# Performance work log

Measured on AMD Instinct MI355X. Metric: run time of the kernel, lower is better.

The kernel has to match this reference:

```python
import jax, jax.numpy as jnp
import numpy as np

EMBED_DIM = 1024
NUM_HEADS = 16
HEAD_DIM = EMBED_DIM // NUM_HEADS
ROPE_BASE = 10000.0
SQK_INIT_VALUE = 1.0
SQK_INIT_SCALING = 1.0 / (EMBED_DIM ** 0.5)


def setup_inputs() -> dict:
    key = jax.random.key(0)
    ks = jax.random.split(key, 6)
    B, N = 1, 2048
    x = jax.random.normal(ks[0], (B, N, EMBED_DIM), dtype=jnp.float32)
    # torch nn.Linear weights are [out_features, in_features]; y = x @ W.T
    s = EMBED_DIM ** -0.5
    Wq = jax.random.normal(ks[1], (EMBED_DIM, EMBED_DIM), dtype=jnp.float32) * s
    Wk = jax.random.normal(ks[2], (EMBED_DIM, EMBED_DIM), dtype=jnp.float32) * s
    Wv = jax.random.normal(ks[3], (EMBED_DIM, EMBED_DIM), dtype=jnp.float32) * s
    Wo = jax.random.normal(ks[4], (EMBED_DIM, EMBED_DIM), dtype=jnp.float32) * s
    sqk = SQK_INIT_SCALING * jnp.ones((EMBED_DIM,), dtype=jnp.float32) \
        + 0.01 * jax.random.normal(ks[5], (EMBED_DIM,), dtype=jnp.float32)
    return {"x": x, "Wq": Wq, "Wk": Wk, "Wv": Wv, "Wo": Wo, "sqk": sqk}


def _rope(t, offset=0):
    # t: [b, h, n, d]; rotary position embedding (Lrpe type 1), half-split layout
    d = t.shape[-1]
    n = t.shape[-2]
    inv_freq = 1.0 / (ROPE_BASE ** (jnp.arange(0, d, 2, dtype=jnp.float32) / d))  # [d/2]
    pos = jnp.arange(n, dtype=jnp.float32) + offset                               # [n]
    freqs = pos[:, None] * inv_freq[None, :]                                      # [n, d/2]
    cos = jnp.cos(freqs)
    sin = jnp.sin(freqs)
    t1, t2 = jnp.split(t, 2, axis=-1)
    return jnp.concatenate([t1 * cos - t2 * sin, t1 * sin + t2 * cos], axis=-1)


def _justnorm(t):
    return t / jnp.linalg.norm(t, axis=-1, keepdims=True)


def reference(x, Wq, Wk, Wv, Wo, sqk):
    B, N, E = x.shape
    H, D = NUM_HEADS, HEAD_DIM
    q = jnp.einsum('bne,fe->bnf', x, Wq).reshape(B, N, H, D).transpose(0, 2, 1, 3)
    k = jnp.einsum('bne,fe->bnf', x, Wk).reshape(B, N, H, D).transpose(0, 2, 1, 3)
    v = jnp.einsum('bne,fe->bnf', x, Wv).reshape(B, N, H, D).transpose(0, 2, 1, 3)
    q = _rope(q)
    k = _rope(k)
    # sqk * (init_value / init_scaling), reshaped to (h, 1, d)
    sqk_s = (sqk * (SQK_INIT_VALUE / SQK_INIT_SCALING)).reshape(H, 1, D)
    q = sqk_s * _justnorm(q)
    k = sqk_s * _justnorm(k)
    # SDPA with scale = sqrt(head_dim) (as in the source), causal
    scale = D ** 0.5
    scores = jnp.einsum('bhnd,bhmd->bhnm', q, k) * scale
    causal = jnp.tril(jnp.ones((N, N), dtype=bool))
    scores = jnp.where(causal, scores, -jnp.inf)
    attn = jax.nn.softmax(scores, axis=-1)
    out = jnp.einsum('bhnm,bhmd->bhnd', attn, v)           # [b,h,n,d]
    out = out.transpose(0, 2, 1, 3).reshape(B, N, E)       # [b,n,e]
    out = jnp.einsum('bne,fe->bnf', out, Wo)
    return out
```

## Files before the change

### kernel.cpp

```cpp
#include <hip/hip_runtime.h>
#include <hip/hip_bf16.h>

typedef float f32x4 __attribute__((ext_vector_type(4)));
typedef __bf16 bf16x8 __attribute__((ext_vector_type(8)));
typedef __bf16 bf16x4 __attribute__((ext_vector_type(4)));

__device__ __forceinline__ void gload_lds16(const __bf16* g, __bf16* l) {
  __builtin_amdgcn_global_load_lds(
      (const __attribute__((address_space(1))) void*)g,
      (__attribute__((address_space(3))) void*)l, 16, 0, 0);
}

__global__ __launch_bounds__(256) void convert_all(
    const float* __restrict__ x, const float* __restrict__ wq,
    const float* __restrict__ wk, const float* __restrict__ wv,
    const float* __restrict__ wo, __bf16* __restrict__ dst)
{
  int t = blockIdx.x * 256 + threadIdx.x;
  const float* src; size_t soff;
  if (t < 262144) { src = x; soff = (size_t)t * 8; }
  else {
    int r = (t - 262144) >> 17;
    src = (r == 0) ? wq : (r == 1) ? wk : (r == 2) ? wv : wo;
    soff = (size_t)((t - 262144) & 131071) * 8;
  }
  float4 f0 = *(const float4*)(src + soff);
  float4 f1 = *(const float4*)(src + soff + 4);
  bf16x8 o;
  o[0]=(__bf16)f0.x; o[1]=(__bf16)f0.y; o[2]=(__bf16)f0.z; o[3]=(__bf16)f0.w;
  o[4]=(__bf16)f1.x; o[5]=(__bf16)f1.y; o[6]=(__bf16)f1.z; o[7]=(__bf16)f1.w;
  *(bf16x8*)(dst + (size_t)t * 8) = o;
}

template <int BM, int BN, int BK, typename OutT, bool ROPE>
__global__ __launch_bounds__(256) void gemm_bt(
    const __bf16* __restrict__ A,
    const __bf16* __restrict__ B0, const __bf16* __restrict__ B1, const __bf16* __restrict__ B2,
    OutT* __restrict__ C0, OutT* __restrict__ C1, OutT* __restrict__ C2,
    int M, int N, int K, const float* __restrict__ sqkp)
{
  const __bf16* B = (blockIdx.z == 0) ? B0 : (blockIdx.z == 1) ? B1 : B2;
  OutT* C = (blockIdx.z == 0) ? C0 : (blockIdx.z == 1) ? C1 : C2;

  constexpr int MT = BM / 32, NT = BN / 32, KK = BK / 32;
  constexpr int CPR = BK / 8;
  constexpr int RPI = 64 / CPR;
  __shared__ __align__(16) __bf16 smem[BM * BK + BN * BK];
  __bf16* As = smem;
  __bf16* Bs = smem + BM * BK;

  const int tid = threadIdx.x, w = tid >> 6, l = tid & 63;
  const int wr = w >> 1, wc = w & 1;
  const int g = l >> 4, c16 = l & 15;
  const int bm = blockIdx.y, bn = blockIdx.x;
  const int lr = l / CPR, lc = l % CPR;

  f32x4 acc[MT][NT] = {};
  const int nk = K / BK;

  for (int kt = 0; kt < nk; ++kt) {
    __syncthreads();
#pragma unroll
    for (int i = w; i < BM / RPI; i += 4) {
      int row = i * RPI + lr;
      int sch = lc ^ (row & 7);
      gload_lds16(A + (size_t)(bm * BM + row) * K + kt * BK + sch * 8, As + i * RPI * BK);
    }
#pragma unroll
    for (int i = w; i < BN / RPI; i += 4) {
      int row = i * RPI + lr;
      int sch = lc ^ (row & 7);
      gload_lds16(B + (size_t)(bn * BN + row) * K + kt * BK + sch * 8, Bs + i * RPI * BK);
    }
    __syncthreads();

#pragma unroll
    for (int kk = 0; kk < KK; ++kk) {
      bf16x8 af[MT], bf[NT];
#pragma unroll
      for (int mt = 0; mt < MT; ++mt) {
        int row = wr * (BM / 2) + mt * 16 + c16;
        af[mt] = *(const bf16x8*)(As + row * BK + (((kk * 4 + g) ^ (row & 7)) * 8));
      }
#pragma unroll
      for (int nt = 0; nt < NT; ++nt) {
        int row = wc * (BN / 2) + nt * 16 + c16;
        bf[nt] = *(const bf16x8*)(Bs + row * BK + (((kk * 4 + g) ^ (row & 7)) * 8));
      }
#pragma unroll
      for (int mt = 0; mt < MT; ++mt)
#pragma unroll
        for (int nt = 0; nt < NT; ++nt)
          acc[mt][nt] = __builtin_amdgcn_mfma_f32_16x16x32_bf16(af[mt], bf[nt], acc[mt][nt], 0, 0, 0);
    }
  }

  bool done = false;
  if constexpr (ROPE) {
    static_assert(!ROPE || (NT == 4 && MT == 2), "ROPE kernel assumes BM=64, BN=128");
    if (blockIdx.z == 2) {
      __syncthreads();
#pragma unroll
      for (int mt = 0; mt < MT; ++mt)
#pragma unroll
        for (int nt = 0; nt < NT; ++nt) {
          bf16x4 pk;
#pragma unroll
          for (int r = 0; r < 4; ++r) pk[r] = (__bf16)acc[mt][nt][r];
          int n0 = wr * 32 + mt * 16 + g * 4;
          int d  = nt * 16 + c16;
          *(bf16x4*)(smem + wc * 4608 + d * 72 + n0) = pk;
        }
      __syncthreads();
#pragma unroll
      for (int j = 0; j < 4; ++j) {
        int idx = tid + j * 256;
        int head = idx >> 9;
        int rem = idx & 511;
        int d = rem >> 3;
        int c8 = (rem & 7) * 8;
        bf16x8 val = *(const bf16x8*)(smem + head * 4608 + d * 72 + c8);
        *(bf16x8*)(C + (size_t)((bn * 2 + head) * 64 + d) * 2048 + bm * 64 + c8) = val;
      }
      done = true;
    } else {
      const bool isQ = (blockIdx.z == 0);
      const int hcol = bn * BN + wc * (BN / 2);
      float sq[4];
#pragma unroll
      for (int nt = 0; nt < 4; ++nt) sq[nt] = sqkp[hcol + nt * 16 + c16] * 32.0f;
      const float QSC = 8.0f * 1.4426950408889634f;
      const float L = 0.415241011860919f;
      const float inv0 = exp2f(-(float)c16 * L);
      const float inv1 = exp2f(-(float)(c16 + 16) * L);
#pragma unroll
      for (int mt = 0; mt < MT; ++mt) {
#pragma unroll
        for (int r = 0; r < 4; ++r) {
          int row = bm * BM + wr * (BM / 2) + mt * 16 + g * 4 + r;
          float s0, c0, s1, c1;
          sincosf((float)row * inv0, &s0, &c0);
          sincosf((float)row * inv1, &s1, &c1);
          float v0 = acc[mt][0][r], v1 = acc[mt][1][r];
          float v2 = acc[mt][2][r], v3 = acc[mt][3][r];
          float n0 = v0 * c0 - v2 * s0;
          float n2 = v0 * s0 + v2 * c0;
          float n1 = v1 * c1 - v3 * s1;
          float n3 = v1 * s1 + v3 * c1;
          float ss = n0 * n0 + n1 * n1 + n2 * n2 + n3 * n3;
#pragma unroll
          for (int m2 = 1; m2 < 16; m2 <<= 1) ss += __shfl_xor(ss, m2, 16);
          float rinv = rsqrtf(ss);
          if (isQ) rinv *= QSC;
          C[(size_t)row * N + hcol +  0 + c16] = (OutT)(n0 * sq[0] * rinv);
          C[(size_t)row * N + hcol + 16 + c16] = (OutT)(n1 * sq[1] * rinv);
          C[(size_t)row * N + hcol + 32 + c16] = (OutT)(n2 * sq[2] * rinv);
          C[(size_t)row * N + hcol + 48 + c16] = (OutT)(n3 * sq[3] * rinv);
        }
      }
      done = true;
    }
  }
  if (!done) {
#pragma unroll
    for (int mt = 0; mt < MT; ++mt)
#pragma unroll
      for (int nt = 0; nt < NT; ++nt)
#pragma unroll
        for (int r = 0; r < 4; ++r) {
          int row = bm * BM + wr * (BM / 2) + mt * 16 + g * 4 + r;
          int col = bn * BN + wc * (BN / 2) + nt * 16 + c16;
          C[(size_t)row * N + col] = (OutT)acc[mt][nt][r];
        }
  }
}

#define STAGE(BUF, KT)                                                         \
  {                                                                            \
    _Pragma("unroll")                                                          \
    for (int p = 0; p < 2; ++p) {                                              \
      int row = srow + p * 32;                                                 \
      int sch = sc ^ (row & 7);                                                \
      gload_lds16(Kg + (size_t)((KT) * 64 + row) * 1024 + h * 64 + sch * 8,    \
                  &Ks[BUF][w * 512 + p * 2048]);                               \
      gload_lds16(Vg + ((size_t)h * 64 + row) * 2048 + (KT) * 64 + sch * 8,    \
                  &Vs[BUF][w * 512 + p * 2048]);                               \
    }                                                                          \
  }

__global__ __launch_bounds__(256, 4) void attn_kernel(
    const __bf16* __restrict__ Qg, const __bf16* __restrict__ Kg,
    const __bf16* __restrict__ Vg, __bf16* __restrict__ Og,
    float* __restrict__ oS, float* __restrict__ lS)
{
  __shared__ __align__(16) __bf16 Ks[2][4096];
  __shared__ __align__(16) __bf16 Vs[2][4096];
  __shared__ __align__(16) __bf16 Ps[4][16 * 72];

  const int b = blockIdx.x;
  int h, qt, kts, kte, sidx;
  if (b < 512) {
    int p = b >> 5;
    qt = 16 + p;
    sidx = (b >> 4) & 1;
    h = b & 15;
    int mid = (qt + 1) >> 1;
    kts = sidx ? mid : 0;
    kte = sidx ? qt : (mid - 1);
  } else {
    qt = 15 - ((b - 512) >> 4);
    h = b & 15;
    kts = 0; kte = qt; sidx = -1;
  }
  const int q0 = qt * 64;

  const int tid = threadIdx.x, w = tid >> 6, l = tid & 63;
  const int g = l >> 4, c16 = l & 15;
  const int srow = tid >> 3;
  const int sc   = tid & 7;

  __bf16* Ps_w = &Ps[w][0];
  const int qig = q0 + w * 16 + c16;

  const __bf16* qbase = Qg + (size_t)qig * 1024 + h * 64 + g * 8;
  const bf16x8 qf0 = *(const bf16x8*)(qbase);
  const bf16x8 qf1 = *(const bf16x8*)(qbase + 32);

  f32x4 o[4] = {};
  float lsum = 0.f;

  STAGE(0, kts)

  for (int kt = kts; kt <= kte; ++kt) {
    const int cur = (kt - kts) & 1;
    __syncthreads();
    if (kt < kte) STAGE(cur ^ 1, kt + 1)

    const __bf16* Kb = Ks[cur];
    const __bf16* Vb = Vs[cur];

    f32x4 s[4] = {};
#pragma unroll
    for (int kjb = 0; kjb < 4; ++kjb) {
      int r = kjb * 16 + c16;
      bf16x8 k0 = *(const bf16x8*)((char*)Kb + r * 128 + ((g ^ (r & 7)) * 16));
      bf16x8 k1 = *(const bf16x8*)((char*)Kb + r * 128 + (((4 + g) ^ (r & 7)) * 16));
      s[kjb] = __builtin_amdgcn_mfma_f32_16x16x32_bf16(k0, qf0, s[kjb], 0, 0, 0);
      s[kjb] = __builtin_amdgcn_mfma_f32_16x16x32_bf16(k1, qf1, s[kjb], 0, 0, 0);
    }

    const bool diag = (kt == qt);
#pragma unroll
    for (int kjb = 0; kjb < 4; ++kjb) {
      bf16x4 pk;
#pragma unroll
      for (int r = 0; r < 4; ++r) {
        float sv = s[kjb][r];
        int kvg = kt * 64 + kjb * 16 + g * 4 + r;
        if (diag && kvg > qig) sv = -1e30f;
        float e = exp2f(sv);
        pk[r] = (__bf16)e;
        lsum += e;
      }
      *(bf16x4*)((char*)Ps_w + c16 * 144 + kjb * 32 + g * 8) = pk;
    }

#pragma unroll
    for (int ks = 0; ks < 2; ++ks) {
      bf16x8 pa = *(const bf16x8*)((char*)Ps_w + c16 * 144 + ks * 64 + g * 16);
#pragma unroll
      for (int nt = 0; nt < 4; ++nt) {
        int r = nt * 16 + c16;
        bf16x8 vb = *(const bf16x8*)((char*)Vb + r * 128 + (((ks * 4 + g) ^ (r & 7)) * 16));
        o[nt] = __builtin_amdgcn_mfma_f32_16x16x32_bf16(pa, vb, o[nt], 0, 0, 0);
      }
    }
  }

  lsum += __shfl_xor(lsum, 16);
  lsum += __shfl_xor(lsum, 32);

  if (sidx < 0) {
    float* lsh = (float*)Ps_w;
    if (g == 0) lsh[c16] = lsum;
    __builtin_amdgcn_s_waitcnt(0);
#pragma unroll
    for (int r = 0; r < 4; ++r) {
      float rinv = 1.0f / lsh[g * 4 + r];
      int qi = q0 + w * 16 + g * 4 + r;
#pragma unroll
      for (int nt = 0; nt < 4; ++nt)
        Og[(size_t)qi * 1024 + h * 64 + nt * 16 + c16] = (__bf16)(o[nt][r] * rinv);
    }
  } else {
    float* oBase = oS + (size_t)sidx * 1024 * 1024;
#pragma unroll
    for (int r = 0; r < 4; ++r) {
      int row = q0 + w * 16 + g * 4 + r - 1024;
#pragma unroll
      for (int nt = 0; nt < 4; ++nt)
        oBase[(size_t)row * 1024 + h * 64 + nt * 16 + c16] = o[nt][r];
    }
    if (g == 0)
      lS[(size_t)sidx * 1024 * 16 + (size_t)(qig - 1024) * 16 + h] = lsum;
  }
}

__global__ __launch_bounds__(256) void merge_halves(
    const float* __restrict__ oS, const float* __restrict__ lS,
    __bf16* __restrict__ Og)
{
  int row = blockIdx.x;
  int col = threadIdx.x * 4;
  int h = col >> 6;
  float lsum = lS[(size_t)row * 16 + h] + lS[(size_t)(1024 + row) * 16 + h];
  float rinv = 1.0f / lsum;
  f32x4 a = *(const f32x4*)(oS + (size_t)row * 1024 + col);
  f32x4 bb = *(const f32x4*)(oS + (size_t)(1024 * 1024) + (size_t)row * 1024 + col);
  f32x4 sum = a + bb;
  bf16x4 ob;
  ob[0] = (__bf16)(sum[0] * rinv); ob[1] = (__bf16)(sum[1] * rinv);
  ob[2] = (__bf16)(sum[2] * rinv); ob[3] = (__bf16)(sum[3] * rinv);
  *(bf16x4*)(Og + (size_t)(1024 + row) * 1024 + col) = ob;
}

extern "C" void kernel_launch(void* const* d_in, const int* in_sizes, int n_in,
                              void* d_out, int out_size, void* d_ws, size_t ws_size,
                              hipStream_t stream) {
  const float* x   = (const float*)d_in[0];
  const float* Wq  = (const float*)d_in[1];
  const float* Wk  = (const float*)d_in[2];
  const float* Wv  = (const float*)d_in[3];
  const float* Wo  = (const float*)d_in[4];
  const float* sqk = (const float*)d_in[5];
  float* out = (float*)d_out;

  __bf16* xb  = (__bf16*)d_ws;
  __bf16* wqb = xb  + (size_t)2048 * 1024;
  __bf16* wkb = wqb + (size_t)1024 * 1024;
  __bf16* wvb = wkb + (size_t)1024 * 1024;
  __bf16* wob = wvb + (size_t)1024 * 1024;
  __bf16* qn  = wob + (size_t)1024 * 1024;
  __bf16* kn  = qn  + (size_t)2048 * 1024;
  __bf16* vtb = kn  + (size_t)2048 * 1024;
  __bf16* og  = vtb + (size_t)2048 * 1024;
  float*  oS  = (float*)(og + (size_t)2048 * 1024);
  float*  lS  = oS + (size_t)2 * 1024 * 1024;

  convert_all<<<3072, 256, 0, stream>>>(x, Wq, Wk, Wv, Wo, xb);
  gemm_bt<64, 128, 128, __bf16, true><<<dim3(8, 32, 3), 256, 0, stream>>>(
      xb, wqb, wkb, wvb, qn, kn, vtb, 2048, 1024, 1024, sqk);
  attn_kernel<<<768, 256, 0, stream>>>(qn, kn, vtb, og, oS, lS);
  merge_halves<<<1024, 256, 0, stream>>>(oS, lS, og);
  gemm_bt<64, 64, 128, float, false><<<dim3(16, 32, 1), 256, 0, stream>>>(
      og, wob, wob, wob, out, out, out, 2048, 1024, 1024, nullptr);
}
```

Baseline: 73.87 us.

## Widen attention KV tile to 128 keys per barrier-synchronized stage

Doubles the K/V tile staged into LDS per loop iteration from 64 to 128 keys, so each key tile needs half as many barriers and pipeline stages. The key-tile ranges for the split and unsplit blocks are recomputed for the new tile size, and V gets a 16-slot XOR swizzle for its 256-byte rows. Shared memory doubles, and launch bounds drop to 2 blocks per CU, which lowers occupancy. Some diagonal tiles now compute a masked half that the 64-wide tiling skipped.

```diff
diff --git a/kernel.cpp b/kernel.cpp
--- a/kernel.cpp
+++ b/kernel.cpp
@@ -175,49 +175,57 @@
   }
 }
 
-#define STAGE(BUF, KT)                                                         \
+#define STAGE(BUF, KT2)                                                        \
   {                                                                            \
     _Pragma("unroll")                                                          \
-    for (int p = 0; p < 2; ++p) {                                              \
+    for (int p = 0; p < 4; ++p) {                      \
       int row = srow + p * 32;                                                 \
       int sch = sc ^ (row & 7);                                                \
-      gload_lds16(Kg + (size_t)((KT) * 64 + row) * 1024 + h * 64 + sch * 8,    \
+      gload_lds16(Kg + (size_t)((KT2) * 128 + row) * 1024 + h * 64 + sch * 8,  \
                   &Ks[BUF][w * 512 + p * 2048]);                               \
-      gload_lds16(Vg + ((size_t)h * 64 + row) * 2048 + (KT) * 64 + sch * 8,    \
+    }                                                                          \
+    _Pragma("unroll")                                                          \
+    for (int p = 0; p < 4; ++p) {                     \
+      int row = srow16 + p * 16;                                               \
+      int sch = sc16 ^ (row & 15);                                             \
+      gload_lds16(Vg + ((size_t)h * 64 + row) * 2048 + (KT2) * 128 + sch * 8,  \
                   &Vs[BUF][w * 512 + p * 2048]);                               \
     }                                                                          \
   }
 
-__global__ __launch_bounds__(256, 4) void attn_kernel(
+__global__ __launch_bounds__(256, 2) void attn_kernel(
     const __bf16* __restrict__ Qg, const __bf16* __restrict__ Kg,
     const __bf16* __restrict__ Vg, __bf16* __restrict__ Og,
     float* __restrict__ oS, float* __restrict__ lS)
 {
-  __shared__ __align__(16) __bf16 Ks[2][4096];
-  __shared__ __align__(16) __bf16 Vs[2][4096];
+  __shared__ __align__(16) __bf16 Ks[2][8192];
+  __shared__ __align__(16) __bf16 Vs[2][8192];
   __shared__ __align__(16) __bf16 Ps[4][16 * 72];
 
   const int b = blockIdx.x;
-  int h, qt, kts, kte, sidx;
+  int h, qt, kts2, kte2, sidx;
   if (b < 512) {
     int p = b >> 5;
     qt = 16 + p;
     sidx = (b >> 4) & 1;
     h = b & 15;
-    int mid = (qt + 1) >> 1;
-    kts = sidx ? mid : 0;
-    kte = sidx ? qt : (mid - 1);
+    int T = (qt + 2) >> 1;
+    int T0 = T >> 1;
+    kts2 = sidx ? T0 : 0;
+    kte2 = sidx ? (T - 1) : (T0 - 1);
   } else {
     qt = 15 - ((b - 512) >> 4);
     h = b & 15;
-    kts = 0; kte = qt; sidx = -1;
+    kts2 = 0; kte2 = ((qt + 2) >> 1) - 1; sidx = -1;
   }
   const int q0 = qt * 64;
 
   const int tid = threadIdx.x, w = tid >> 6, l = tid & 63;
   const int g = l >> 4, c16 = l & 15;
-  const int srow = tid >> 3;
-  const int sc   = tid & 7;
+  const int srow   = tid >> 3;
+  const int sc     = tid & 7;
+  const int srow16 = tid >> 4;
+  const int sc16   = tid & 15;
 
   __bf16* Ps_w = &Ps[w][0];
   const int qig = q0 + w * 16 + c16;
@@ -229,50 +237,54 @@
   f32x4 o[4] = {};
   float lsum = 0.f;
 
-  STAGE(0, kts)
-
-  for (int kt = kts; kt <= kte; ++kt) {
-    const int cur = (kt - kts) & 1;
+  STAGE(0, kts2)
+
+  for (int kt2 = kts2; kt2 <= kte2; ++kt2) {
+    const int cur = (kt2 - kts2) & 1;
     __syncthreads();
-    if (kt < kte) STAGE(cur ^ 1, kt + 1)
+    if (kt2 < kte2) STAGE(cur ^ 1, kt2 + 1)
 
     const __bf16* Kb = Ks[cur];
     const __bf16* Vb = Vs[cur];
-
-    f32x4 s[4] = {};
-#pragma unroll
-    for (int kjb = 0; kjb < 4; ++kjb) {
-      int r = kjb * 16 + c16;
-      bf16x8 k0 = *(const bf16x8*)((char*)Kb + r * 128 + ((g ^ (r & 7)) * 16));
-      bf16x8 k1 = *(const bf16x8*)((char*)Kb + r * 128 + (((4 + g) ^ (r & 7)) * 16));
-      s[kjb] = __builtin_amdgcn_mfma_f32_16x16x32_bf16(k0, qf0, s[kjb], 0, 0, 0);
-      s[kjb] = __builtin_amdgcn_mfma_f32_16x16x32_bf16(k1, qf1, s[kjb], 0, 0, 0);
-    }
-
-    const bool diag = (kt == qt);
-#pragma unroll
-    for (int kjb = 0; kjb < 4; ++kjb) {
-      bf16x4 pk;
-#pragma unroll
-      for (int r = 0; r < 4; ++r) {
-        float sv = s[kjb][r];
-        int kvg = kt * 64 + kjb * 16 + g * 4 + r;
-        if (diag && kvg > qig) sv = -1e30f;
-        float e = exp2f(sv);
-        pk[r] = (__bf16)e;
-        lsum += e;
-      }
-      *(bf16x4*)((char*)Ps_w + c16 * 144 + kjb * 32 + g * 8) = pk;
-    }
-
-#pragma unroll
-    for (int ks = 0; ks < 2; ++ks) {
-      bf16x8 pa = *(const bf16x8*)((char*)Ps_w + c16 * 144 + ks * 64 + g * 16);
-#pragma unroll
-      for (int nt = 0; nt < 4; ++nt) {
-        int r = nt * 16 + c16;
-        bf16x8 vb = *(const bf16x8*)((char*)Vb + r * 128 + (((ks * 4 + g) ^ (r & 7)) * 16));
-        o[nt] = __builtin_amdgcn_mfma_f32_16x16x32_bf16(pa, vb, o[nt], 0, 0, 0);
+    const bool diag = (kt2 == ((qt >> 1)));
+
+#pragma unroll
+    for (int su = 0; su < 2; ++su) {
+      f32x4 s[4] = {};
+#pragma unroll
+      for (int kjb = 0; kjb < 4; ++kjb) {
+        int r = su * 64 + kjb * 16 + c16;
+        bf16x8 k0 = *(const bf16x8*)((char*)Kb + r * 128 + ((g ^ (r & 7)) * 16));
+        bf16x8 k1 = *(const bf16x8*)((char*)Kb + r * 128 + (((4 + g) ^ (r & 7)) * 16));
+        s[kjb] = __builtin_amdgcn_mfma_f32_16x16x32_bf16(k0, qf0, s[kjb], 0, 0, 0);
+        s[kjb] = __builtin_amdgcn_mfma_f32_16x16x32_bf16(k1, qf1, s[kjb], 0, 0, 0);
+      }
+
+#pragma unroll
+      for (int kjb = 0; kjb < 4; ++kjb) {
+        bf16x4 pk;
+#pragma unroll
+        for (int r = 0; r < 4; ++r) {
+          float sv = s[kjb][r];
+          int kvg = kt2 * 128 + su * 64 + kjb * 16 + g * 4 + r;
+          if (diag && kvg > qig) sv = -1e30f;
+          float e = exp2f(sv);
+          pk[r] = (__bf16)e;
+          lsum += e;
+        }
+        *(bf16x4*)((char*)Ps_w + c16 * 144 + kjb * 32 + g * 8) = pk;
+      }
+
+#pragma unroll
+      for (int ks = 0; ks < 2; ++ks) {
+        bf16x8 pa = *(const bf16x8*)((char*)Ps_w + c16 * 144 + ks * 64 + g * 16);
+#pragma unroll
+        for (int nt = 0; nt < 4; ++nt) {
+          int r = nt * 16 + c16;
+          int slot = (su * 8 + ks * 4 + g) ^ (r & 15);
+          bf16x8 vb = *(const bf16x8*)((char*)Vb + r * 256 + slot * 16);
+          o[nt] = __builtin_amdgcn_mfma_f32_16x16x32_bf16(pa, vb, o[nt], 0, 0, 0);
+        }
       }
     }
   }
```

After: 77.97 us, median of 2. 5.5% more time.

## Use 128-row query tiles with 512 threads and split KV into up to 3 chunks

Applied to the files above, without the earlier changes.

The attention kernel now processes 128 query rows per block with 8 waves sharing each staged K/V tile, which halves the K/V loads per query. Long query tiles are split across the KV range into 3 chunks (middle tiles into 2), and a generalized merge kernel combines the partial outputs. This should improve K/V reuse and balance work across CUs. In exchange, the causal mask is now applied on every tile, the partial-output workspace grows, and the merge pass reads more data.

```diff
diff --git a/kernel.cpp b/kernel.cpp
--- a/kernel.cpp
+++ b/kernel.cpp
@@ -177,47 +177,45 @@
 
 #define STAGE(BUF, KT)                                                         \
   {                                                                            \
-    _Pragma("unroll")                                                          \
-    for (int p = 0; p < 2; ++p) {                                              \
-      int row = srow + p * 32;                                                 \
-      int sch = sc ^ (row & 7);                                                \
-      gload_lds16(Kg + (size_t)((KT) * 64 + row) * 1024 + h * 64 + sch * 8,    \
-                  &Ks[BUF][w * 512 + p * 2048]);                               \
-      gload_lds16(Vg + ((size_t)h * 64 + row) * 2048 + (KT) * 64 + sch * 8,    \
-                  &Vs[BUF][w * 512 + p * 2048]);                               \
-    }                                                                          \
-  }
-
-__global__ __launch_bounds__(256, 4) void attn_kernel(
+    int row_ = w * 8 + (l >> 3);                                               \
+    int sch_ = (l & 7) ^ (row_ & 7);                                           \
+    gload_lds16(Kg + (size_t)((KT) * 64 + row_) * 1024 + h * 64 + sch_ * 8,    \
+                &Ks[BUF][w * 512]);                                            \
+    gload_lds16(Vg + ((size_t)h * 64 + row_) * 2048 + (KT) * 64 + sch_ * 8,    \
+                &Vs[BUF][w * 512]);                                            \
+  }
+
+__global__ __launch_bounds__(512, 6) void attn_kernel(
     const __bf16* __restrict__ Qg, const __bf16* __restrict__ Kg,
     const __bf16* __restrict__ Vg, __bf16* __restrict__ Og,
     float* __restrict__ oS, float* __restrict__ lS)
 {
   __shared__ __align__(16) __bf16 Ks[2][4096];
   __shared__ __align__(16) __bf16 Vs[2][4096];
-  __shared__ __align__(16) __bf16 Ps[4][16 * 72];
+  __shared__ __align__(16) __bf16 Ps[8][16 * 72];
 
   const int b = blockIdx.x;
-  int h, qt, kts, kte, sidx;
-  if (b < 512) {
-    int p = b >> 5;
-    qt = 16 + p;
-    sidx = (b >> 4) & 1;
-    h = b & 15;
-    int mid = (qt + 1) >> 1;
-    kts = sidx ? mid : 0;
-    kte = sidx ? qt : (mid - 1);
+  int h, qt2, kts, kte, sidx, nsp;
+  if (b < 384) {
+    qt2 = 15 - b / 48;
+    int idx = b % 48;
+    sidx = idx >> 4; nsp = 3; h = idx & 15;
+  } else if (b < 512) {
+    int t = b - 384;
+    qt2 = 7 - t / 32;
+    sidx = (t >> 4) & 1; nsp = 2; h = t & 15;
   } else {
-    qt = 15 - ((b - 512) >> 4);
-    h = b & 15;
-    kts = 0; kte = qt; sidx = -1;
-  }
-  const int q0 = qt * 64;
+    int t = b - 512;
+    qt2 = 3 - (t >> 4);
+    sidx = -1; nsp = 1; h = t & 15;
+  }
+  const int T = 2 * qt2 + 2;
+  if (sidx < 0) { kts = 0; kte = T - 1; }
+  else          { kts = sidx * T / nsp; kte = (sidx + 1) * T / nsp - 1; }
+  const int q0 = qt2 * 128;
 
   const int tid = threadIdx.x, w = tid >> 6, l = tid & 63;
   const int g = l >> 4, c16 = l & 15;
-  const int srow = tid >> 3;
-  const int sc   = tid & 7;
 
   __bf16* Ps_w = &Ps[w][0];
   const int qig = q0 + w * 16 + c16;
@@ -249,7 +247,6 @@
       s[kjb] = __builtin_amdgcn_mfma_f32_16x16x32_bf16(k1, qf1, s[kjb], 0, 0, 0);
     }
 
-    const bool diag = (kt == qt);
 #pragma unroll
     for (int kjb = 0; kjb < 4; ++kjb) {
       bf16x4 pk;
@@ -257,7 +254,7 @@
       for (int r = 0; r < 4; ++r) {
         float sv = s[kjb][r];
         int kvg = kt * 64 + kjb * 16 + g * 4 + r;
-        if (diag && kvg > qig) sv = -1e30f;
+        if (kvg > qig) sv = -1e30f;
         float e = exp2f(sv);
         pk[r] = (__bf16)e;
         lsum += e;
@@ -293,35 +290,39 @@
         Og[(size_t)qi * 1024 + h * 64 + nt * 16 + c16] = (__bf16)(o[nt][r] * rinv);
     }
   } else {
-    float* oBase = oS + (size_t)sidx * 1024 * 1024;
+    float* oBase = oS + (size_t)sidx * 2048 * 1024;
 #pragma unroll
     for (int r = 0; r < 4; ++r) {
-      int row = q0 + w * 16 + g * 4 + r - 1024;
+      int row = q0 + w * 16 + g * 4 + r;
 #pragma unroll
       for (int nt = 0; nt < 4; ++nt)
         oBase[(size_t)row * 1024 + h * 64 + nt * 16 + c16] = o[nt][r];
     }
     if (g == 0)
-      lS[(size_t)sidx * 1024 * 16 + (size_t)(qig - 1024) * 16 + h] = lsum;
-  }
-}
-
-__global__ __launch_bounds__(256) void merge_halves(
+      lS[(size_t)sidx * 2048 * 16 + (size_t)qig * 16 + h] = lsum;
+  }
+}
+
+__global__ __launch_bounds__(256) void merge_chunks(
     const float* __restrict__ oS, const float* __restrict__ lS,
     __bf16* __restrict__ Og)
 {
-  int row = blockIdx.x;
+  int row = 512 + blockIdx.x;
   int col = threadIdx.x * 4;
   int h = col >> 6;
-  float lsum = lS[(size_t)row * 16 + h] + lS[(size_t)(1024 + row) * 16 + h];
+  int nch = (row < 1024) ? 2 : 3;
+  float lsum = 0.f;
+  f32x4 sum = {};
+#pragma unroll 3
+  for (int c = 0; c < nch; ++c) {
+    lsum += lS[(size_t)c * 2048 * 16 + (size_t)row * 16 + h];
+    sum += *(const f32x4*)(oS + (size_t)c * 2048 * 1024 + (size_t)row * 1024 + col);
+  }
   float rinv = 1.0f / lsum;
-  f32x4 a = *(const f32x4*)(oS + (size_t)row * 1024 + col);
-  f32x4 bb = *(const f32x4*)(oS + (size_t)(1024 * 1024) + (size_t)row * 1024 + col);
-  f32x4 sum = a + bb;
   bf16x4 ob;
   ob[0] = (__bf16)(sum[0] * rinv); ob[1] = (__bf16)(sum[1] * rinv);
   ob[2] = (__bf16)(sum[2] * rinv); ob[3] = (__bf16)(sum[3] * rinv);
-  *(bf16x4*)(Og + (size_t)(1024 + row) * 1024 + col) = ob;
+  *(bf16x4*)(Og + (size_t)row * 1024 + col) = ob;
 }
 
 extern "C" void kernel_launch(void* const* d_in, const int* in_sizes, int n_in,
@@ -345,13 +346,13 @@
   __bf16* vtb = kn  + (size_t)2048 * 1024;
   __bf16* og  = vtb + (size_t)2048 * 1024;
   float*  oS  = (float*)(og + (size_t)2048 * 1024);
-  float*  lS  = oS + (size_t)2 * 1024 * 1024;
+  float*  lS  = oS + (size_t)3 * 2048 * 1024;
 
   convert_all<<<3072, 256, 0, stream>>>(x, Wq, Wk, Wv, Wo, xb);
   gemm_bt<64, 128, 128, __bf16, true><<<dim3(8, 32, 3), 256, 0, stream>>>(
       xb, wqb, wkb, wvb, qn, kn, vtb, 2048, 1024, 1024, sqk);
-  attn_kernel<<<768, 256, 0, stream>>>(qn, kn, vtb, og, oS, lS);
-  merge_halves<<<1024, 256, 0, stream>>>(oS, lS, og);
+  attn_kernel<<<576, 512, 0, stream>>>(qn, kn, vtb, og, oS, lS);
+  merge_chunks<<<1536, 256, 0, stream>>>(oS, lS, og);
   gemm_bt<64, 64, 128, float, false><<<dim3(16, 32, 1), 256, 0, stream>>>(
       og, wob, wob, wob, out, out, out, 2048, 1024, 1024, nullptr);
 }
```

Measured after the change: 75.84 us. 2.7% more time.
